# Kernel optimization log

Measured on AMD Instinct MI355X. Metric: run time of the kernel, lower is better.

The kernel has to match this reference:

```python
import jax, jax.numpy as jnp
import numpy as np

DIM = 1024
NUM_HEADS = 16
HEAD_DIM = DIM // NUM_HEADS
SCALE = HEAD_DIM ** -0.5


def setup_inputs() -> dict:
    key0 = jax.random.key(0)
    ks = jax.random.split(key0, 8)
    B, L, S = 2, 1024, 2048
    inp = {
        "query": jax.random.normal(ks[0], (B, L, DIM), dtype=jnp.float32),
        "key": jax.random.normal(ks[1], (B, S, DIM), dtype=jnp.float32),
        "value": jax.random.normal(ks[2], (B, S, DIM), dtype=jnp.float32),
        # projection weights, stored as [in, out] so x @ W matches torch Linear
        "Wq": jax.random.normal(ks[3], (DIM, DIM), dtype=jnp.float32) * (DIM ** -0.5),
        "Wk": jax.random.normal(ks[4], (DIM, DIM), dtype=jnp.float32) * (DIM ** -0.5),
        "Wv": jax.random.normal(ks[5], (DIM, DIM), dtype=jnp.float32) * (DIM ** -0.5),
        "Wo": jax.random.normal(ks[6], (DIM, DIM), dtype=jnp.float32) * (DIM ** -0.5),
        "bo": jax.random.normal(ks[7], (DIM,), dtype=jnp.float32) * 0.02,
    }
    return inp


def reference(query, key, value, Wq, Wk, Wv, Wo, bo):
    B, L, C = query.shape
    S = key.shape[1]
    H, D = NUM_HEADS, HEAD_DIM
    # QKV projections (no bias), split heads: [B, H, L/S, D]
    q = (query @ Wq).reshape(B, L, H, D).transpose(0, 2, 1, 3)
    k = (key @ Wk).reshape(B, S, H, D).transpose(0, 2, 1, 3)
    v = (value @ Wv).reshape(B, S, H, D).transpose(0, 2, 1, 3)
    # scaled dot-product attention (qk_norm=False -> identity)
    attn = jnp.einsum("bhld,bhsd->bhls", q * SCALE, k)
    attn = jax.nn.softmax(attn, axis=-1)
    x = jnp.einsum("bhls,bhsd->bhld", attn, v)
    x = x.transpose(0, 2, 1, 3).reshape(B, L, C)
    # output projection (with bias)
    return x @ Wo + bo
```

## Files before the change

kernel.cpp:

```cpp
#include <hip/hip_runtime.h>

namespace {

typedef _Float16 f16;
typedef __attribute__((ext_vector_type(4))) _Float16 f16x4;
typedef __attribute__((ext_vector_type(8))) _Float16 f16x8;
typedef __attribute__((ext_vector_type(4))) float f32x4;

constexpr int kDim   = 1024;
constexpr int kHeads = 16;
constexpr int kHd    = 64;
constexpr int kB     = 2;
constexpr int kL     = 1024;
constexpr int kS     = 2048;

struct PrepArgs {
  const float* csrc[3];
  f16* cdst[3];
  int cn[3];
  const float* w[4];
  f16* wt[4];
};

__global__ __launch_bounds__(256) void prep(PrepArgs a) {
  __shared__ float T[32][33];
  const int y = blockIdx.y;
  if (y < 3) {
    const int i = (blockIdx.x * 256 + threadIdx.x) * 8;
    if (i >= a.cn[y]) return;
    const float* __restrict__ src = a.csrc[y];
    float4 v0 = *(const float4*)(src + i);
    float4 v1 = *(const float4*)(src + i + 4);
    f16x8 h = {(f16)v0.x, (f16)v0.y, (f16)v0.z, (f16)v0.w,
               (f16)v1.x, (f16)v1.y, (f16)v1.z, (f16)v1.w};
    *(f16x8*)(a.cdst[y] + i) = h;
  } else {
    if (blockIdx.x >= 1024) return;
    const int z = y - 3;
    const float* __restrict__ W = a.w[z];
    f16* __restrict__ Wt = a.wt[z];
    const int n0 = (blockIdx.x & 31) * 32;
    const int k0 = (blockIdx.x >> 5) * 32;
    const int r = threadIdx.x >> 3;
    const int c = (threadIdx.x & 7) * 4;
    float4 v = *(const float4*)(W + (size_t)(k0 + r) * kDim + n0 + c);
    T[c + 0][r] = v.x; T[c + 1][r] = v.y; T[c + 2][r] = v.z; T[c + 3][r] = v.w;
    __syncthreads();
    f16x4 h = {(f16)T[r][c], (f16)T[r][c + 1], (f16)T[r][c + 2], (f16)T[r][c + 3]};
    *(f16x4*)(Wt + (size_t)(n0 + r) * kDim + k0 + c) = h;
  }
}

struct ProjArgs {
  const f16* A[3];
  const f16* Bt[3];
  f16* C[3];
};

__global__ __launch_bounds__(256) void gemm_proj(ProjArgs p) {
  constexpr int K = kDim;
  constexpr int NI = K / 32;
  int bx = blockIdx.x;
  int z, m0, n0, Nz;
  if (bx < 128)      { z = 0; m0 = (bx >> 3) * 128; n0 = (bx & 7) * 128; Nz = kDim; }
  else if (bx < 384) { bx -= 128; z = 1; m0 = (bx >> 3) * 128; n0 = (bx & 7) * 128; Nz = kDim; }
  else               { bx -= 384; z = 2; m0 = (bx >> 5) * 128; n0 = (bx & 31) * 128; Nz = kB * kS; }
  const f16* __restrict__ A  = p.A[z];
  const f16* __restrict__ Bt = p.Bt[z];
  f16* __restrict__ C = p.C[z];

  __shared__ __align__(16) f16 As[2][128 * 32];
  __shared__ __align__(16) f16 Bs[2][128 * 32];
  const int t = threadIdx.x;
  const int lane = t & 63;
  const int wave = t >> 6;
  const int wm = (wave >> 1) * 64;
  const int wn = (wave & 1) * 64;
  const int col = lane & 15;
  const int quad = lane >> 4;

  f32x4 acc[4][4];
#pragma unroll
  for (int i = 0; i < 4; ++i)
#pragma unroll
    for (int j = 0; j < 4; ++j) acc[i][j] = (f32x4){0.f, 0.f, 0.f, 0.f};

  const int c0 = t, c1 = t + 256;
  const f16* a0 = A + (size_t)(m0 + (c0 >> 2)) * K + (c0 & 3) * 8;
  const f16* a1 = A + (size_t)(m0 + (c1 >> 2)) * K + (c1 & 3) * 8;
  const f16* b0 = Bt + (size_t)(n0 + (c0 >> 2)) * K + (c0 & 3) * 8;
  const f16* b1 = Bt + (size_t)(n0 + (c1 >> 2)) * K + (c1 & 3) * 8;

  {
    f16x8 ra0 = *(const f16x8*)(a0);
    f16x8 ra1 = *(const f16x8*)(a1);
    f16x8 rb0 = *(const f16x8*)(b0);
    f16x8 rb1 = *(const f16x8*)(b1);
    *(f16x8*)(As[0] + c0 * 8) = ra0;
    *(f16x8*)(As[0] + c1 * 8) = ra1;
    *(f16x8*)(Bs[0] + c0 * 8) = rb0;
    *(f16x8*)(Bs[0] + c1 * 8) = rb1;
  }

  for (int i = 0; i < NI; ++i) {
    const int cur = i & 1;
    f16x8 na0, na1, nb0, nb1;
    if (i + 1 < NI) {
      const int ko = (i + 1) * 32;
      na0 = *(const f16x8*)(a0 + ko);
      na1 = *(const f16x8*)(a1 + ko);
      nb0 = *(const f16x8*)(b0 + ko);
      nb1 = *(const f16x8*)(b1 + ko);
    }
    __syncthreads();

    f16x8 af[4], bf[4];
#pragma unroll
    for (int mt = 0; mt < 4; ++mt)
      af[mt] = *(const f16x8*)(As[cur] + (wm + mt * 16 + col) * 32 + quad * 8);
#pragma unroll
    for (int nt = 0; nt < 4; ++nt)
      bf[nt] = *(const f16x8*)(Bs[cur] + (wn + nt * 16 + col) * 32 + quad * 8);
#pragma unroll
    for (int mt = 0; mt < 4; ++mt)
#pragma unroll
      for (int nt = 0; nt < 4; ++nt)
        acc[mt][nt] = __builtin_amdgcn_mfma_f32_16x16x32_f16(
            af[mt], bf[nt], acc[mt][nt], 0, 0, 0);

    if (i + 1 < NI) {
      const int nxt = 1 - cur;
      *(f16x8*)(As[nxt] + c0 * 8) = na0;
      *(f16x8*)(As[nxt] + c1 * 8) = na1;
      *(f16x8*)(Bs[nxt] + c0 * 8) = nb0;
      *(f16x8*)(Bs[nxt] + c1 * 8) = nb1;
    }
  }

  const int crow = m0 + wm + quad * 4;
  const int ccol = n0 + wn + col;
#pragma unroll
  for (int mt = 0; mt < 4; ++mt)
#pragma unroll
    for (int nt = 0; nt < 4; ++nt)
#pragma unroll
      for (int r = 0; r < 4; ++r)
        C[(size_t)(crow + mt * 16 + r) * Nz + ccol + nt * 16] =
            (f16)acc[mt][nt][r];
}

__global__ __launch_bounds__(256) void gemm_out(
    const f16* __restrict__ A, const f16* __restrict__ Bt,
    const float* __restrict__ bias, float* __restrict__ C, int M, int N, int K)
{
  __shared__ __align__(16) f16 As[2][64 * 32];
  __shared__ __align__(16) f16 Bs[2][64 * 32];
  const int t = threadIdx.x;
  const int lane = t & 63;
  const int wave = t >> 6;
  const int n0 = blockIdx.x * 64;
  const int m0 = blockIdx.y * 64;
  const int wm = (wave >> 1) * 32;
  const int wn = (wave & 1) * 32;
  const int col = lane & 15;
  const int quad = lane >> 4;
  const int NI = K / 32;

  f32x4 acc[2][2];
#pragma unroll
  for (int i = 0; i < 2; ++i)
#pragma unroll
    for (int j = 0; j < 2; ++j) acc[i][j] = (f32x4){0.f, 0.f, 0.f, 0.f};

  const f16* a0 = A + (size_t)(m0 + (t >> 2)) * K + (t & 3) * 8;
  const f16* b0 = Bt + (size_t)(n0 + (t >> 2)) * K + (t & 3) * 8;

  {
    f16x8 ra0 = *(const f16x8*)(a0);
    f16x8 rb0 = *(const f16x8*)(b0);
    *(f16x8*)(As[0] + t * 8) = ra0;
    *(f16x8*)(Bs[0] + t * 8) = rb0;
  }

  for (int i = 0; i < NI; ++i) {
    const int cur = i & 1;
    f16x8 na0, nb0;
    if (i + 1 < NI) {
      const int ko = (i + 1) * 32;
      na0 = *(const f16x8*)(a0 + ko);
      nb0 = *(const f16x8*)(b0 + ko);
    }
    __syncthreads();

    f16x8 af[2], bf[2];
#pragma unroll
    for (int mt = 0; mt < 2; ++mt)
      af[mt] = *(const f16x8*)(As[cur] + (wm + mt * 16 + col) * 32 + quad * 8);
#pragma unroll
    for (int nt = 0; nt < 2; ++nt)
      bf[nt] = *(const f16x8*)(Bs[cur] + (wn + nt * 16 + col) * 32 + quad * 8);
#pragma unroll
    for (int mt = 0; mt < 2; ++mt)
#pragma unroll
      for (int nt = 0; nt < 2; ++nt)
        acc[mt][nt] = __builtin_amdgcn_mfma_f32_16x16x32_f16(
            af[mt], bf[nt], acc[mt][nt], 0, 0, 0);

    if (i + 1 < NI) {
      const int nxt = 1 - cur;
      *(f16x8*)(As[nxt] + t * 8) = na0;
      *(f16x8*)(Bs[nxt] + t * 8) = nb0;
    }
  }

  const int crow = m0 + wm + quad * 4;
  const int ccol = n0 + wn + col;
#pragma unroll
  for (int mt = 0; mt < 2; ++mt)
#pragma unroll
    for (int nt = 0; nt < 2; ++nt) {
      const float bv = bias[ccol + nt * 16];
#pragma unroll
      for (int r = 0; r < 4; ++r)
        C[(size_t)(crow + mt * 16 + r) * N + ccol + nt * 16] =
            acc[mt][nt][r] + bv;
    }
}

__global__ __launch_bounds__(256) void flash_attn_mfma3(
    const f16* __restrict__ q, const f16* __restrict__ k,
    const f16* __restrict__ vT, f16* __restrict__ x)
{
  constexpr int LP = 72;
  constexpr int NT = kS / 64;
  __shared__ __align__(16) f16 Kt[2][64 * LP];
  __shared__ __align__(16) f16 Vt[2][64 * LP];
  __shared__ __align__(16) f16 Pb[4][16 * LP];

  const int t    = threadIdx.x;
  const int lane = t & 63;
  const int wave = t >> 6;
  const int col  = lane & 15;
  const int quad = lane >> 4;
  const int bh   = blockIdx.x;
  const int l0   = blockIdx.y * 64;
  const int h    = bh & (kHeads - 1);
  const int b    = bh >> 4;

  f16* Pw = Pb[wave];

  f16x8 qf[2];
  {
    const f16* src = q + ((size_t)b * kL + l0 + wave * 16 + col) * kDim + h * kHd;
    qf[0] = *(const f16x8*)(src + quad * 8);
    qf[1] = *(const f16x8*)(src + 32 + quad * 8);
#pragma unroll
    for (int u = 0; u < 8; ++u) {
      qf[0][u] = qf[0][u] * (f16)0.125f;
      qf[1][u] = qf[1][u] * (f16)0.125f;
    }
  }

  const int sr = t >> 2;
  const int sc = (t & 3) * 16;
  const f16* kbase = k + ((size_t)b * kS + sr) * kDim + h * kHd + sc;
  const f16* vbase = vT + ((size_t)(h * kHd + sr)) * (kB * kS) + b * kS + sc;

  float l_part[4];
  f32x4 accO[4];
#pragma unroll
  for (int r = 0; r < 4; ++r) l_part[r] = 0.f;
#pragma unroll
  for (int dt = 0; dt < 4; ++dt) accO[dt] = (f32x4){0.f, 0.f, 0.f, 0.f};

  {
    f16x8 k0v = *(const f16x8*)(kbase);
    f16x8 k1v = *(const f16x8*)(kbase + 8);
    f16x8 v0v = *(const f16x8*)(vbase);
    f16x8 v1v = *(const f16x8*)(vbase + 8);
    *(f16x8*)(Kt[0] + sr * LP + sc)     = k0v;
    *(f16x8*)(Kt[0] + sr * LP + sc + 8) = k1v;
    *(f16x8*)(Vt[0] + sr * LP + sc)     = v0v;
    *(f16x8*)(Vt[0] + sr * LP + sc + 8) = v1v;
  }

  for (int i = 0; i < NT; ++i) {
    const int cur = i & 1;
    f16x8 nk0, nk1, nv0, nv1;
    if (i + 1 < NT) {
      const f16* kn = kbase + (size_t)(i + 1) * 64 * kDim;
      const f16* vn = vbase + (i + 1) * 64;
      nk0 = *(const f16x8*)(kn);
      nk1 = *(const f16x8*)(kn + 8);
      nv0 = *(const f16x8*)(vn);
      nv1 = *(const f16x8*)(vn + 8);
    }
    __syncthreads();

    f32x4 s4[4];
#pragma unroll
    for (int ns = 0; ns < 4; ++ns) s4[ns] = (f32x4){0.f, 0.f, 0.f, 0.f};
#pragma unroll
    for (int ns = 0; ns < 4; ++ns) {
      f16x8 kf0 = *(const f16x8*)(Kt[cur] + (ns * 16 + col) * LP + quad * 8);
      f16x8 kf1 = *(const f16x8*)(Kt[cur] + (ns * 16 + col) * LP + 32 + quad * 8);
      s4[ns] = __builtin_amdgcn_mfma_f32_16x16x32_f16(qf[0], kf0, s4[ns], 0, 0, 0);
      s4[ns] = __builtin_amdgcn_mfma_f32_16x16x32_f16(qf[1], kf1, s4[ns], 0, 0, 0);
    }

#pragma unroll
    for (int r = 0; r < 4; ++r) {
      float rs = 0.f;
#pragma unroll
      for (int ns = 0; ns < 4; ++ns) {
        float pv = __expf(s4[ns][r]);
        Pw[(quad * 4 + r) * LP + ns * 16 + col] = (f16)pv;
        rs += pv;
      }
      l_part[r] += rs;
    }

    f16x8 pf0 = *(const f16x8*)(Pw + col * LP + quad * 8);
    f16x8 pf1 = *(const f16x8*)(Pw + col * LP + 32 + quad * 8);
#pragma unroll
    for (int dt = 0; dt < 4; ++dt) {
      f16x8 vf0 = *(const f16x8*)(Vt[cur] + (dt * 16 + col) * LP + quad * 8);
      f16x8 vf1 = *(const f16x8*)(Vt[cur] + (dt * 16 + col) * LP + 32 + quad * 8);
      accO[dt] = __builtin_amdgcn_mfma_f32_16x16x32_f16(pf0, vf0, accO[dt], 0, 0, 0);
      accO[dt] = __builtin_amdgcn_mfma_f32_16x16x32_f16(pf1, vf1, accO[dt], 0, 0, 0);
    }

    if (i + 1 < NT) {
      const int nxt = 1 - cur;
      *(f16x8*)(Kt[nxt] + sr * LP + sc)     = nk0;
      *(f16x8*)(Kt[nxt] + sr * LP + sc + 8) = nk1;
      *(f16x8*)(Vt[nxt] + sr * LP + sc)     = nv0;
      *(f16x8*)(Vt[nxt] + sr * LP + sc + 8) = nv1;
    }
  }

#pragma unroll
  for (int r = 0; r < 4; ++r) {
    float lv = l_part[r];
    lv += __shfl_xor(lv, 1, 16);
    lv += __shfl_xor(lv, 2, 16);
    lv += __shfl_xor(lv, 4, 16);
    lv += __shfl_xor(lv, 8, 16);
    const float inv = 1.f / lv;
    const size_t row = (size_t)b * kL + l0 + wave * 16 + quad * 4 + r;
#pragma unroll
    for (int dt = 0; dt < 4; ++dt)
      x[row * kDim + h * kHd + dt * 16 + col] = (f16)(accO[dt][r] * inv);
  }
}

}

extern "C" void kernel_launch(void* const* d_in, const int* in_sizes, int n_in,
                              void* d_out, int out_size, void* d_ws, size_t ws_size,
                              hipStream_t stream) {
  const float* query = (const float*)d_in[0];
  const float* key   = (const float*)d_in[1];
  const float* value = (const float*)d_in[2];
  const float* Wq    = (const float*)d_in[3];
  const float* Wk    = (const float*)d_in[4];
  const float* Wv    = (const float*)d_in[5];
  const float* Wo    = (const float*)d_in[6];
  const float* bo    = (const float*)d_in[7];
  float* out = (float*)d_out;

  f16* ws = (f16*)d_ws;
  f16* qh  = ws;
  f16* kh  = qh + (size_t)kB * kL * kDim;
  f16* vh  = kh + (size_t)kB * kS * kDim;
  f16* wqt = vh + (size_t)kB * kS * kDim;
  f16* wkt = wqt + (size_t)kDim * kDim;
  f16* wvt = wkt + (size_t)kDim * kDim;
  f16* wot = wvt + (size_t)kDim * kDim;
  f16* qp  = wot + (size_t)kDim * kDim;
  f16* kp  = qp + (size_t)kB * kL * kDim;
  f16* vpT = kp + (size_t)kB * kS * kDim;
  f16* xh  = vpT + (size_t)kB * kS * kDim;

  PrepArgs pr;
  pr.csrc[0] = query; pr.cdst[0] = qh; pr.cn[0] = kB * kL * kDim;
  pr.csrc[1] = key;   pr.cdst[1] = kh; pr.cn[1] = kB * kS * kDim;
  pr.csrc[2] = value; pr.cdst[2] = vh; pr.cn[2] = kB * kS * kDim;
  pr.w[0] = Wq; pr.wt[0] = wqt;
  pr.w[1] = Wk; pr.wt[1] = wkt;
  pr.w[2] = Wv; pr.wt[2] = wvt;
  pr.w[3] = Wo; pr.wt[3] = wot;
  prep<<<dim3(2048, 7), 256, 0, stream>>>(pr);

  ProjArgs pa;
  pa.A[0] = qh;  pa.Bt[0] = wqt; pa.C[0] = qp;
  pa.A[1] = kh;  pa.Bt[1] = wkt; pa.C[1] = kp;
  pa.A[2] = wvt; pa.Bt[2] = vh;  pa.C[2] = vpT;
  gemm_proj<<<dim3(640), 256, 0, stream>>>(pa);

  flash_attn_mfma3<<<dim3(kB * kHeads, kL / 64), 256, 0, stream>>>(
      qp, kp, vpT, xh);

  gemm_out<<<dim3(kDim / 64, (kB * kL) / 64), 256, 0, stream>>>(
      xh, wot, bo, out, kB * kL, kDim, kDim);
}
```

Baseline: 196.9 us.

## Rewrite flash attention with 32x32 MFMA, split-KV waves, and register-resident P

Recasts the attention kernel to use 32x32x16 MFMA tiles. S^T is computed so that P can be repacked into the A operand in registers via v_permlane32_swap, which drops the LDS round trip for P. The four waves are split into two query halves times two KV halves, each pair covering half of the sequence, with partial outputs and row sums reduced through LDS at the end. It also adds s_setprio around the MFMA blocks and launch_bounds(256,2). In exchange it doubles LDS staging per block and adds higher register pressure plus a final cross-wave reduction.

New measurement: 178.1 us. 1.11x faster.

```diff
diff --git a/kernel.cpp b/kernel.cpp
--- a/kernel.cpp
+++ b/kernel.cpp
@@ -3,9 +3,11 @@
 namespace {
 
 typedef _Float16 f16;
+typedef __attribute__((ext_vector_type(2))) _Float16 f16x2;
 typedef __attribute__((ext_vector_type(4))) _Float16 f16x4;
 typedef __attribute__((ext_vector_type(8))) _Float16 f16x8;
 typedef __attribute__((ext_vector_type(4))) float f32x4;
+typedef __attribute__((ext_vector_type(16))) float f32x16;
 
 constexpr int kDim   = 1024;
 constexpr int kHeads = 16;
@@ -227,130 +229,171 @@
     }
 }
 
-__global__ __launch_bounds__(256) void flash_attn_mfma3(
+
+__device__ inline unsigned pk2f(float a, float b) {
+  union { f16x2 h; unsigned u; } c;
+  c.h = f16x2{(f16)a, (f16)b};
+  return c.u;
+}
+
+__device__ inline void swap32(unsigned& x, unsigned& y) {
+  asm("v_permlane32_swap_b32 %0, %1" : "+v"(x), "+v"(y));
+}
+
+__global__ __launch_bounds__(256, 2) void flash_attn_mfma4(
     const f16* __restrict__ q, const f16* __restrict__ k,
     const f16* __restrict__ vT, f16* __restrict__ x)
 {
-  constexpr int LP = 72;
-  constexpr int NT = kS / 64;
-  __shared__ __align__(16) f16 Kt[2][64 * LP];
-  __shared__ __align__(16) f16 Vt[2][64 * LP];
-  __shared__ __align__(16) f16 Pb[4][16 * LP];
+  constexpr int LP  = 72;
+  constexpr int NT2 = (kS / 2) / 64;
+  __shared__ __align__(16) f16 Kt[2][2][64 * LP];
+  __shared__ __align__(16) f16 Vt[2][2][64 * LP];
 
   const int t    = threadIdx.x;
   const int lane = t & 63;
   const int wave = t >> 6;
-  const int col  = lane & 15;
-  const int quad = lane >> 4;
+  const int wq   = wave & 1;
+  const int wh   = wave >> 1;
+  const int ln   = lane & 31;
+  const int hi   = lane >> 5;
   const int bh   = blockIdx.x;
   const int l0   = blockIdx.y * 64;
   const int h    = bh & (kHeads - 1);
   const int b    = bh >> 4;
 
-  f16* Pw = Pb[wave];
-
-  f16x8 qf[2];
+  f16x8 qf[4];
   {
-    const f16* src = q + ((size_t)b * kL + l0 + wave * 16 + col) * kDim + h * kHd;
-    qf[0] = *(const f16x8*)(src + quad * 8);
-    qf[1] = *(const f16x8*)(src + 32 + quad * 8);
-#pragma unroll
-    for (int u = 0; u < 8; ++u) {
-      qf[0][u] = qf[0][u] * (f16)0.125f;
-      qf[1][u] = qf[1][u] * (f16)0.125f;
-    }
-  }
-
-  const int sr = t >> 2;
-  const int sc = (t & 3) * 16;
-  const f16* kbase = k + ((size_t)b * kS + sr) * kDim + h * kHd + sc;
-  const f16* vbase = vT + ((size_t)(h * kHd + sr)) * (kB * kS) + b * kS + sc;
-
-  float l_part[4];
-  f32x4 accO[4];
-#pragma unroll
-  for (int r = 0; r < 4; ++r) l_part[r] = 0.f;
-#pragma unroll
-  for (int dt = 0; dt < 4; ++dt) accO[dt] = (f32x4){0.f, 0.f, 0.f, 0.f};
-
-  {
-    f16x8 k0v = *(const f16x8*)(kbase);
-    f16x8 k1v = *(const f16x8*)(kbase + 8);
-    f16x8 v0v = *(const f16x8*)(vbase);
-    f16x8 v1v = *(const f16x8*)(vbase + 8);
-    *(f16x8*)(Kt[0] + sr * LP + sc)     = k0v;
-    *(f16x8*)(Kt[0] + sr * LP + sc + 8) = k1v;
-    *(f16x8*)(Vt[0] + sr * LP + sc)     = v0v;
-    *(f16x8*)(Vt[0] + sr * LP + sc + 8) = v1v;
-  }
-
-  for (int i = 0; i < NT; ++i) {
+    const f16* src = q + ((size_t)b * kL + l0 + wq * 32 + ln) * kDim + h * kHd + hi * 8;
+#pragma unroll
+    for (int ks = 0; ks < 4; ++ks) {
+      qf[ks] = *(const f16x8*)(src + ks * 16);
+#pragma unroll
+      for (int u = 0; u < 8; ++u) qf[ks][u] *= (f16)0.125f;
+    }
+  }
+
+  const int srow = t >> 2;
+  const int scol = (t & 3) * 16;
+  const f16* kb = k + ((size_t)b * kS + srow) * kDim + h * kHd + scol;
+  const f16* vb = vT + ((size_t)(h * kHd + srow)) * (kB * kS) + b * kS + scol;
+  const size_t kHalf = (size_t)1024 * kDim;
+
+  f32x16 accO[2];
+#pragma unroll
+  for (int dt = 0; dt < 2; ++dt)
+#pragma unroll
+    for (int r = 0; r < 16; ++r) accO[dt][r] = 0.f;
+  float lsum = 0.f;
+
+  f16x8 kh0a, kh0b, kh1a, kh1b, vh0a, vh0b, vh1a, vh1b;
+
+#define STAGE_LOAD(i)                                                   \
+  { const f16* kp0 = kb + (size_t)(i) * 64 * kDim;                      \
+    const f16* kp1 = kp0 + kHalf;                                       \
+    const f16* vp0 = vb + (i) * 64;                                     \
+    const f16* vp1 = vp0 + 1024;                                        \
+    kh0a = *(const f16x8*)(kp0); kh0b = *(const f16x8*)(kp0 + 8);       \
+    kh1a = *(const f16x8*)(kp1); kh1b = *(const f16x8*)(kp1 + 8);       \
+    vh0a = *(const f16x8*)(vp0); vh0b = *(const f16x8*)(vp0 + 8);       \
+    vh1a = *(const f16x8*)(vp1); vh1b = *(const f16x8*)(vp1 + 8); }
+
+#define STAGE_WRITE(bf)                                                 \
+  { f16* kd0 = &Kt[bf][0][srow * LP + scol];                            \
+    f16* kd1 = &Kt[bf][1][srow * LP + scol];                            \
+    f16* vd0 = &Vt[bf][0][srow * LP + scol];                            \
+    f16* vd1 = &Vt[bf][1][srow * LP + scol];                            \
+    *(f16x8*)(kd0) = kh0a; *(f16x8*)(kd0 + 8) = kh0b;                   \
+    *(f16x8*)(kd1) = kh1a; *(f16x8*)(kd1 + 8) = kh1b;                   \
+    *(f16x8*)(vd0) = vh0a; *(f16x8*)(vd0 + 8) = vh0b;                   \
+    *(f16x8*)(vd1) = vh1a; *(f16x8*)(vd1 + 8) = vh1b; }
+
+  STAGE_LOAD(0);
+  STAGE_WRITE(0);
+
+  for (int i = 0; i < NT2; ++i) {
     const int cur = i & 1;
-    f16x8 nk0, nk1, nv0, nv1;
-    if (i + 1 < NT) {
-      const f16* kn = kbase + (size_t)(i + 1) * 64 * kDim;
-      const f16* vn = vbase + (i + 1) * 64;
-      nk0 = *(const f16x8*)(kn);
-      nk1 = *(const f16x8*)(kn + 8);
-      nv0 = *(const f16x8*)(vn);
-      nv1 = *(const f16x8*)(vn + 8);
-    }
+    if (i + 1 < NT2) STAGE_LOAD(i + 1);
     __syncthreads();
 
-    f32x4 s4[4];
-#pragma unroll
-    for (int ns = 0; ns < 4; ++ns) s4[ns] = (f32x4){0.f, 0.f, 0.f, 0.f};
-#pragma unroll
-    for (int ns = 0; ns < 4; ++ns) {
-      f16x8 kf0 = *(const f16x8*)(Kt[cur] + (ns * 16 + col) * LP + quad * 8);
-      f16x8 kf1 = *(const f16x8*)(Kt[cur] + (ns * 16 + col) * LP + 32 + quad * 8);
-      s4[ns] = __builtin_amdgcn_mfma_f32_16x16x32_f16(qf[0], kf0, s4[ns], 0, 0, 0);
-      s4[ns] = __builtin_amdgcn_mfma_f32_16x16x32_f16(qf[1], kf1, s4[ns], 0, 0, 0);
-    }
-
-#pragma unroll
-    for (int r = 0; r < 4; ++r) {
-      float rs = 0.f;
-#pragma unroll
-      for (int ns = 0; ns < 4; ++ns) {
-        float pv = __expf(s4[ns][r]);
-        Pw[(quad * 4 + r) * LP + ns * 16 + col] = (f16)pv;
-        rs += pv;
+    const f16* Kc = &Kt[cur][wh][0];
+    const f16* Vc = &Vt[cur][wh][0];
+
+    f16x8 pf[4];
+#pragma unroll
+    for (int sub = 0; sub < 2; ++sub) {
+      f32x16 s;
+#pragma unroll
+      for (int r = 0; r < 16; ++r) s[r] = 0.f;
+      __builtin_amdgcn_s_setprio(1);
+#pragma unroll
+      for (int ks = 0; ks < 4; ++ks) {
+        f16x8 kf = *(const f16x8*)(Kc + (sub * 32 + ln) * LP + ks * 16 + hi * 8);
+        s = __builtin_amdgcn_mfma_f32_32x32x16_f16(kf, qf[ks], s, 0, 0, 0);
       }
-      l_part[r] += rs;
-    }
-
-    f16x8 pf0 = *(const f16x8*)(Pw + col * LP + quad * 8);
-    f16x8 pf1 = *(const f16x8*)(Pw + col * LP + 32 + quad * 8);
-#pragma unroll
-    for (int dt = 0; dt < 4; ++dt) {
-      f16x8 vf0 = *(const f16x8*)(Vt[cur] + (dt * 16 + col) * LP + quad * 8);
-      f16x8 vf1 = *(const f16x8*)(Vt[cur] + (dt * 16 + col) * LP + 32 + quad * 8);
-      accO[dt] = __builtin_amdgcn_mfma_f32_16x16x32_f16(pf0, vf0, accO[dt], 0, 0, 0);
-      accO[dt] = __builtin_amdgcn_mfma_f32_16x16x32_f16(pf1, vf1, accO[dt], 0, 0, 0);
-    }
-
-    if (i + 1 < NT) {
-      const int nxt = 1 - cur;
-      *(f16x8*)(Kt[nxt] + sr * LP + sc)     = nk0;
-      *(f16x8*)(Kt[nxt] + sr * LP + sc + 8) = nk1;
-      *(f16x8*)(Vt[nxt] + sr * LP + sc)     = nv0;
-      *(f16x8*)(Vt[nxt] + sr * LP + sc + 8) = nv1;
-    }
-  }
-
-#pragma unroll
-  for (int r = 0; r < 4; ++r) {
-    float lv = l_part[r];
-    lv += __shfl_xor(lv, 1, 16);
-    lv += __shfl_xor(lv, 2, 16);
-    lv += __shfl_xor(lv, 4, 16);
-    lv += __shfl_xor(lv, 8, 16);
-    const float inv = 1.f / lv;
-    const size_t row = (size_t)b * kL + l0 + wave * 16 + quad * 4 + r;
-#pragma unroll
-    for (int dt = 0; dt < 4; ++dt)
-      x[row * kDim + h * kHd + dt * 16 + col] = (f16)(accO[dt][r] * inv);
+      __builtin_amdgcn_s_setprio(0);
+
+      float pp[16];
+#pragma unroll
+      for (int r = 0; r < 16; ++r) { pp[r] = __expf(s[r]); lsum += pp[r]; }
+
+#pragma unroll
+      for (int kk = 0; kk < 2; ++kk) {
+        unsigned a0 = pk2f(pp[8 * kk + 0], pp[8 * kk + 1]);
+        unsigned a1 = pk2f(pp[8 * kk + 2], pp[8 * kk + 3]);
+        unsigned b0 = pk2f(pp[8 * kk + 4], pp[8 * kk + 5]);
+        unsigned b1 = pk2f(pp[8 * kk + 6], pp[8 * kk + 7]);
+        swap32(a0, b0);
+        swap32(a1, b1);
+        union { unsigned u[4]; f16x8 v; } w;
+        w.u[0] = a0; w.u[1] = a1; w.u[2] = b0; w.u[3] = b1;
+        pf[sub * 2 + kk] = w.v;
+      }
+    }
+
+    __builtin_amdgcn_s_setprio(1);
+#pragma unroll
+    for (int dt = 0; dt < 2; ++dt)
+#pragma unroll
+      for (int ks = 0; ks < 4; ++ks) {
+        f16x8 vf = *(const f16x8*)(Vc + (dt * 32 + ln) * LP + ks * 16 + hi * 8);
+        accO[dt] = __builtin_amdgcn_mfma_f32_32x32x16_f16(pf[ks], vf, accO[dt], 0, 0, 0);
+      }
+    __builtin_amdgcn_s_setprio(0);
+
+    if (i + 1 < NT2) STAGE_WRITE(1 - cur);
+  }
+#undef STAGE_LOAD
+#undef STAGE_WRITE
+
+  lsum += __shfl_xor(lsum, 32);
+  __syncthreads();
+  float* sc = (float*)&Kt[0][0][0];
+  float* sl = sc + 128 * 33;
+  if (wh == 1) {
+    float* dst = sc + (wq * 64 + lane) * 33;
+#pragma unroll
+    for (int dt = 0; dt < 2; ++dt)
+#pragma unroll
+      for (int r = 0; r < 16; ++r) dst[dt * 16 + r] = accO[dt][r];
+    sl[wq * 64 + lane] = lsum;
+  }
+  __syncthreads();
+  if (wh == 0) {
+    const float* src = sc + (wq * 64 + lane) * 33;
+#pragma unroll
+    for (int dt = 0; dt < 2; ++dt)
+#pragma unroll
+      for (int r = 0; r < 16; ++r) accO[dt][r] += src[dt * 16 + r];
+    const float inv = 1.f / (lsum + sl[wq * 64 + lane]);
+    const size_t row0 = (size_t)b * kL + l0 + wq * 32;
+    f16* xb = x + row0 * kDim + h * kHd + ln;
+#pragma unroll
+    for (int r = 0; r < 16; ++r) {
+      const int qr = (r & 3) + 8 * (r >> 2) + 4 * hi;
+      const float invr = __shfl(inv, qr);
+      xb[(size_t)qr * kDim]      = (f16)(accO[0][r] * invr);
+      xb[(size_t)qr * kDim + 32] = (f16)(accO[1][r] * invr);
+    }
   }
 }
 
@@ -398,7 +441,7 @@
   pa.A[2] = wvt; pa.Bt[2] = vh;  pa.C[2] = vpT;
   gemm_proj<<<dim3(640), 256, 0, stream>>>(pa);
 
-  flash_attn_mfma3<<<dim3(kB * kHeads, kL / 64), 256, 0, stream>>>(
+  flash_attn_mfma4<<<dim3(kB * kHeads, kL / 64), 256, 0, stream>>>(
       qp, kp, vpT, xh);
 
   gemm_out<<<dim3(kDim / 64, (kB * kL) / 64), 256, 0, stream>>>(
```
